# Kernel tuning notes

Measured on AMD Instinct MI355X. Metric: run time of the kernel, lower is better.

## Reference

```python
import jax, jax.numpy as jnp
import numpy as np

D = 1024

def setup_inputs() -> dict:
    key = jax.random.key(0)
    ks = jax.random.split(key, 7)
    s = 1.0 / np.sqrt(D)
    x = jax.random.normal(ks[0], (4, 4096, D), dtype=jnp.float32)
    Wi = jax.random.uniform(ks[1], (2 * D, D), jnp.float32, -s, s)   # in_proj weight [2D, D]
    bi = jax.random.uniform(ks[2], (2 * D,), jnp.float32, -s, s)
    Wc = jax.random.uniform(ks[3], (D, 1, 3), jnp.float32, -0.577, 0.577)  # depthwise conv [D,1,3]
    bc = jax.random.uniform(ks[4], (D,), jnp.float32, -0.577, 0.577)
    Wo = jax.random.uniform(ks[5], (D, D), jnp.float32, -s, s)       # out_proj weight [D, D]
    bo = jax.random.uniform(ks[6], (D,), jnp.float32, -s, s)
    return {"x": x, "Wi": Wi, "bi": bi, "Wc": Wc, "bc": bc, "Wo": Wo, "bo": bo}

def _depthwise_conv1d(v, Wc, bc):
    # v: [B, L, D] -> NCH [B, D, L]; kernel [D, 1, 3] (OIH), groups = D; pad 1 both sides
    y = jax.lax.conv_general_dilated(
        v.transpose(0, 2, 1), Wc,
        window_strides=(1,), padding=[(1, 1)],
        dimension_numbers=("NCH", "OIH", "NCH"),
        feature_group_count=v.shape[-1])
    return y.transpose(0, 2, 1) + bc  # [B, L, D]

def reference(x, Wi, bi, Wc, bc, Wo, bo):
    uv = jnp.einsum("bld,ed->ble", x, Wi) + bi        # [B, L, 2D]
    u, v = jnp.split(uv, 2, axis=-1)                   # each [B, L, D]
    y = _depthwise_conv1d(v, Wc, bc)
    y = jax.nn.silu(y) * u                             # fused gate
    return jnp.einsum("bld,ed->ble", y, Wo) + bo       # [B, L, D]
```

## Files before the change

### kernel.cpp

```cpp
#include <hip/hip_runtime.h>
#include <math.h>


typedef __attribute__((ext_vector_type(8))) short short8;
typedef __attribute__((ext_vector_type(4))) float floatx4;

__device__ __forceinline__ float b2f(short s) {
    unsigned int u = ((unsigned int)(unsigned short)s) << 16;
    float f;
    __builtin_memcpy(&f, &u, 4);
    return f;
}

__device__ __forceinline__ short f2b(float f) {
    unsigned int u;
    __builtin_memcpy(&u, &f, 4);
    u += 0x7fffu + ((u >> 16) & 1u);
    return (short)(u >> 16);
}

__device__ __forceinline__ void gl_lds16(const short* g, short* l) {
    __builtin_amdgcn_global_load_lds(
        (const __attribute__((address_space(1))) unsigned int*)g,
        (__attribute__((address_space(3))) unsigned int*)l,
        16, 0, 0);
}

__global__ __launch_bounds__(256) void cvt_all(
    const float* __restrict__ x, const float* __restrict__ Wi,
    const float* __restrict__ Wo, short* __restrict__ xb,
    short* __restrict__ Wib, short* __restrict__ Wob)
{
    constexpr int n1 = 16384 * 1024 / 8;
    constexpr int n2 = 2048 * 1024 / 8;
    constexpr int n3 = 1024 * 1024 / 8;
    int i = blockIdx.x * 256 + threadIdx.x;
    const float* src;
    short* dst;
    int j;
    if (i < n1)           { src = x;  dst = xb;  j = i; }
    else if (i < n1 + n2) { src = Wi; dst = Wib; j = i - n1; }
    else if (i < n1 + n2 + n3) { src = Wo; dst = Wob; j = i - n1 - n2; }
    else return;
    float4 a = ((const float4*)src)[2 * j];
    float4 b = ((const float4*)src)[2 * j + 1];
    short8 o;
    o[0] = f2b(a.x); o[1] = f2b(a.y); o[2] = f2b(a.z); o[3] = f2b(a.w);
    o[4] = f2b(b.x); o[5] = f2b(b.y); o[6] = f2b(b.z); o[7] = f2b(b.w);
    ((short8*)dst)[j] = o;
}

template <bool OUTF32>
__global__ __launch_bounds__(256, 2) void gemm_bt(
    const short* __restrict__ A, const short* __restrict__ B,
    const float* __restrict__ bias, void* __restrict__ Cv,
    int lda, int ldb, int ldc)
{
    constexpr int K = 1024;
    __shared__ __attribute__((aligned(16))) short As[128 * 32];
    __shared__ __attribute__((aligned(16))) short Bs[128 * 32];

    const int tid  = threadIdx.x;
    const int wave = tid >> 6;
    const int lane = tid & 63;
    const int mBase = blockIdx.x * 128;
    const int nBase = blockIdx.y * 128;

    floatx4 acc[4][4];
#pragma unroll
    for (int i = 0; i < 4; i++)
#pragma unroll
        for (int j = 0; j < 4; j++) acc[i][j] = {0.f, 0.f, 0.f, 0.f};

    const int sRow = wave * 32 + (lane >> 2);
    const int sCol = (((lane & 3) ^ ((lane >> 3) & 3))) * 8;
    const short* gA = A + (size_t)(mBase + sRow) * lda + sCol;
    const short* gB = B + (size_t)(nBase + sRow) * ldb + sCol;
    short* lA = &As[(wave * 32) * 32];
    short* lB = &Bs[(wave * 32) * 32];

    const int mq = (wave & 1) * 64;
    const int nq = (wave >> 1) * 64;
    const int fRow = lane & 15;
    const int lg   = lane >> 4;
    const int swz  = (fRow >> 1) & 3;
    const int fOff = (lg ^ swz) * 8;

    for (int k0 = 0; k0 < K; k0 += 32) {
        __syncthreads();
        gl_lds16(gA + k0,            lA);
        gl_lds16(gA + 16 * lda + k0, lA + 16 * 32);
        gl_lds16(gB + k0,            lB);
        gl_lds16(gB + 16 * ldb + k0, lB + 16 * 32);
        __syncthreads();

        short8 a[4], b[4];
#pragma unroll
        for (int mi = 0; mi < 4; mi++)
            a[mi] = *(const short8*)&As[(mq + mi * 16 + fRow) * 32 + fOff];
#pragma unroll
        for (int ni = 0; ni < 4; ni++)
            b[ni] = *(const short8*)&Bs[(nq + ni * 16 + fRow) * 32 + fOff];
#pragma unroll
        for (int mi = 0; mi < 4; mi++)
#pragma unroll
            for (int ni = 0; ni < 4; ni++)
                acc[mi][ni] = __builtin_amdgcn_mfma_f32_16x16x32_bf16(
                    a[mi], b[ni], acc[mi][ni], 0, 0, 0);
    }

    const int colq = lane & 15;
    const int rowq = (lane >> 4) * 4;
#pragma unroll
    for (int ni = 0; ni < 4; ni++) {
        const int col = nBase + nq + ni * 16 + colq;
        const float bv = bias[col];
#pragma unroll
        for (int mi = 0; mi < 4; mi++) {
            const int row = mBase + mq + mi * 16 + rowq;
#pragma unroll
            for (int r = 0; r < 4; r++) {
                float v = acc[mi][ni][r] + bv;
                if (OUTF32)
                    ((float*)Cv)[(size_t)(row + r) * ldc + col] = v;
                else
                    ((short*)Cv)[(size_t)(row + r) * ldc + col] = f2b(v);
            }
        }
    }
}

__global__ __launch_bounds__(256) void conv_gate(
    const short* __restrict__ uv, const float* __restrict__ Wc,
    const float* __restrict__ bc, short* __restrict__ yb)
{
    const int idx = blockIdx.x * 256 + threadIdx.x;
    const int d8 = idx & 127;
    const int m  = idx >> 7;
    const int l  = m & 4095;
    const int d  = d8 * 8;

    float w[24];
#pragma unroll
    for (int q = 0; q < 6; q++)
        *(float4*)&w[q * 4] = ((const float4*)(Wc + d * 3))[q];
    float bcv[8];
    *(float4*)&bcv[0] = ((const float4*)(bc + d))[0];
    *(float4*)&bcv[4] = ((const float4*)(bc + d))[1];

    const size_t rowu = (size_t)m * 2048 + d;
    const size_t rowv = rowu + 1024;

    const short8 z = {0, 0, 0, 0, 0, 0, 0, 0};
    const short8 us = *(const short8*)(uv + rowu);
    const short8 vc = *(const short8*)(uv + rowv);
    const short8 vm = (l > 0)    ? *(const short8*)(uv + rowv - 2048) : z;
    const short8 vp = (l < 4095) ? *(const short8*)(uv + rowv + 2048) : z;

    short8 outv;
#pragma unroll
    for (int j = 0; j < 8; j++) {
        float y = b2f(vm[j]) * w[j * 3 + 0]
                + b2f(vc[j]) * w[j * 3 + 1]
                + b2f(vp[j]) * w[j * 3 + 2]
                + bcv[j];
        float sil = y / (1.0f + expf(-y));
        outv[j] = f2b(sil * b2f(us[j]));
    }
    *(short8*)(yb + (size_t)m * 1024 + d) = outv;
}

extern "C" void kernel_launch(void* const* d_in, const int* in_sizes, int n_in,
                              void* d_out, int out_size, void* d_ws, size_t ws_size,
                              hipStream_t stream)
{
    const float* x  = (const float*)d_in[0];
    const float* Wi = (const float*)d_in[1];
    const float* bi = (const float*)d_in[2];
    const float* Wc = (const float*)d_in[3];
    const float* bc = (const float*)d_in[4];
    const float* Wo = (const float*)d_in[5];
    const float* bo = (const float*)d_in[6];
    float* out = (float*)d_out;

    short* wsS = (short*)d_ws;
    short* uv  = wsS;
    short* xb  = uv + (size_t)16384 * 2048;
    short* Wib = xb + (size_t)16384 * 1024;
    short* Wob = Wib + (size_t)2048 * 1024;

    dim3 blk(256);

    constexpr int nCvt = (16384 * 1024 + 2048 * 1024 + 1024 * 1024) / 8;
    cvt_all<<<(nCvt + 255) / 256, blk, 0, stream>>>(x, Wi, Wo, xb, Wib, Wob);

    dim3 g1(16384 / 128, 2048 / 128);
    gemm_bt<false><<<g1, blk, 0, stream>>>(xb, Wib, bi, uv, 1024, 1024, 2048);

    conv_gate<<<(16384 * 128) / 256, blk, 0, stream>>>(uv, Wc, bc, xb);

    dim3 g2(16384 / 128, 1024 / 128);
    gemm_bt<true><<<g2, blk, 0, stream>>>(xb, Wob, bo, out, 1024, 1024, 1024);
}
```

Baseline: 297.6 us.

## Double GEMM K-tile to 64 with 8-way LDS swizzle and N-major grid

The GEMM K step grows from 32 to 64, so each tile now needs half as many barrier pairs, and the LDS XOR swizzle is widened to 8 groups to suit the 128-byte rows. The grid is swapped so blockIdx.x walks N, meaning consecutive blocks share the same A rows, which should improve L2 reuse of the activation matrix. Launch bounds go from 2 to 3 blocks per CU to raise occupancy. The cost is double the LDS per block (32 KB) and a tighter register budget, which may cause spills or limit how many blocks actually fit.

```diff
diff --git a/kernel.cpp b/kernel.cpp
--- a/kernel.cpp
+++ b/kernel.cpp
@@ -51,20 +51,20 @@
 }
 
 template <bool OUTF32>
-__global__ __launch_bounds__(256, 2) void gemm_bt(
+__global__ __launch_bounds__(256, 3) void gemm_bt(
     const short* __restrict__ A, const short* __restrict__ B,
     const float* __restrict__ bias, void* __restrict__ Cv,
     int lda, int ldb, int ldc)
 {
     constexpr int K = 1024;
-    __shared__ __attribute__((aligned(16))) short As[128 * 32];
-    __shared__ __attribute__((aligned(16))) short Bs[128 * 32];
+    __shared__ __attribute__((aligned(16))) short As[128 * 64];
+    __shared__ __attribute__((aligned(16))) short Bs[128 * 64];
 
     const int tid  = threadIdx.x;
     const int wave = tid >> 6;
     const int lane = tid & 63;
-    const int mBase = blockIdx.x * 128;
-    const int nBase = blockIdx.y * 128;
+    const int mBase = blockIdx.y * 128;
+    const int nBase = blockIdx.x * 128;
 
     floatx4 acc[4][4];
 #pragma unroll
@@ -72,41 +72,45 @@
 #pragma unroll
         for (int j = 0; j < 4; j++) acc[i][j] = {0.f, 0.f, 0.f, 0.f};
 
-    const int sRow = wave * 32 + (lane >> 2);
-    const int sCol = (((lane & 3) ^ ((lane >> 3) & 3))) * 8;
-    const short* gA = A + (size_t)(mBase + sRow) * lda + sCol;
-    const short* gB = B + (size_t)(nBase + sRow) * ldb + sCol;
-    short* lA = &As[(wave * 32) * 32];
-    short* lB = &Bs[(wave * 32) * 32];
+    const int sRow = wave * 32 + (lane >> 3);
+    const int sg   = (((lane & 7) ^ ((lane >> 3) & 7))) * 8;
+    const short* gA = A + (size_t)(mBase + sRow) * lda + sg;
+    const short* gB = B + (size_t)(nBase + sRow) * ldb + sg;
+    short* lA = &As[(wave * 32) * 64];
+    short* lB = &Bs[(wave * 32) * 64];
 
     const int mq = (wave & 1) * 64;
     const int nq = (wave >> 1) * 64;
     const int fRow = lane & 15;
     const int lg   = lane >> 4;
-    const int swz  = (fRow >> 1) & 3;
-    const int fOff = (lg ^ swz) * 8;
-
-    for (int k0 = 0; k0 < K; k0 += 32) {
+    const int p0   = ((lg ^ (fRow & 7))) * 8;
+
+    for (int k0 = 0; k0 < K; k0 += 64) {
         __syncthreads();
-        gl_lds16(gA + k0,            lA);
-        gl_lds16(gA + 16 * lda + k0, lA + 16 * 32);
-        gl_lds16(gB + k0,            lB);
-        gl_lds16(gB + 16 * ldb + k0, lB + 16 * 32);
+#pragma unroll
+        for (int j = 0; j < 4; j++) {
+            gl_lds16(gA + (size_t)(8 * j) * lda + k0, lA + 8 * j * 64);
+            gl_lds16(gB + (size_t)(8 * j) * ldb + k0, lB + 8 * j * 64);
+        }
         __syncthreads();
 
-        short8 a[4], b[4];
-#pragma unroll
-        for (int mi = 0; mi < 4; mi++)
-            a[mi] = *(const short8*)&As[(mq + mi * 16 + fRow) * 32 + fOff];
-#pragma unroll
-        for (int ni = 0; ni < 4; ni++)
-            b[ni] = *(const short8*)&Bs[(nq + ni * 16 + fRow) * 32 + fOff];
-#pragma unroll
-        for (int mi = 0; mi < 4; mi++)
+#pragma unroll
+        for (int h = 0; h < 2; h++) {
+            const int po = p0 ^ (h * 32);
+            short8 a[4], b[4];
+#pragma unroll
+            for (int mi = 0; mi < 4; mi++)
+                a[mi] = *(const short8*)&As[(mq + mi * 16 + fRow) * 64 + po];
 #pragma unroll
             for (int ni = 0; ni < 4; ni++)
-                acc[mi][ni] = __builtin_amdgcn_mfma_f32_16x16x32_bf16(
-                    a[mi], b[ni], acc[mi][ni], 0, 0, 0);
+                b[ni] = *(const short8*)&Bs[(nq + ni * 16 + fRow) * 64 + po];
+#pragma unroll
+            for (int mi = 0; mi < 4; mi++)
+#pragma unroll
+                for (int ni = 0; ni < 4; ni++)
+                    acc[mi][ni] = __builtin_amdgcn_mfma_f32_16x16x32_bf16(
+                        a[mi], b[ni], acc[mi][ni], 0, 0, 0);
+        }
     }
 
     const int colq = lane & 15;
@@ -194,11 +198,11 @@
     constexpr int nCvt = (16384 * 1024 + 2048 * 1024 + 1024 * 1024) / 8;
     cvt_all<<<(nCvt + 255) / 256, blk, 0, stream>>>(x, Wi, Wo, xb, Wib, Wob);
 
-    dim3 g1(16384 / 128, 2048 / 128);
+    dim3 g1(2048 / 128, 16384 / 128);
     gemm_bt<false><<<g1, blk, 0, stream>>>(xb, Wib, bi, uv, 1024, 1024, 2048);
 
     conv_gate<<<(16384 * 128) / 256, blk, 0, stream>>>(uv, Wc, bc, xb);
 
-    dim3 g2(16384 / 128, 1024 / 128);
+    dim3 g2(1024 / 128, 16384 / 128);
     gemm_bt<true><<<g2, blk, 0, stream>>>(xb, Wob, bo, out, 1024, 1024, 1024);
 }
```

Result: faster. 281.9 us (-5.3%).
